# Kernel tuning notes

Hardware: AMD Instinct MI355X
Metric: run time of the kernel (lower is better)

## Reference

```python
import jax, jax.numpy as jnp
import numpy as np

B, N, D, H = 2, 2048, 1024, 16
HD = D // H
SCALE = 1.0 / float(np.sqrt(HD))


def _cx(r, i):
    return (r + 1j * i).astype(jnp.complex64)


def setup_inputs() -> dict:
    key = jax.random.key(0)
    ks = jax.random.split(key, 20)
    inp = {
        "Z_r": jax.random.normal(ks[0], (B, N, D), jnp.float32),
        "Z_i": jax.random.normal(ks[1], (B, N, D), jnp.float32),
    }
    i = 2
    w_scale = 0.02
    for nm in ("q", "k", "v", "o"):
        inp[f"w{nm}_r"] = jax.random.normal(ks[i], (D, D), jnp.float32) * w_scale
        inp[f"w{nm}_i"] = jax.random.normal(ks[i + 1], (D, D), jnp.float32) * w_scale
        inp[f"b{nm}_r"] = jax.random.normal(ks[i + 2], (D,), jnp.float32) * w_scale
        inp[f"b{nm}_i"] = jax.random.normal(ks[i + 3], (D,), jnp.float32) * w_scale
        i += 4
    inp["mask"] = jax.random.randint(ks[18], (B, N), 0, 2, jnp.int32)
    return inp


def reference(Z_r, Z_i, wq_r, wq_i, bq_r, bq_i, wk_r, wk_i, bk_r, bk_i,
              wv_r, wv_i, bv_r, bv_i, wo_r, wo_i, bo_r, bo_i, mask):
    Z = _cx(Z_r, Z_i)  # (B,N,D) complex64

    def lin(x, wr, wi, br, bi):  # complex nn.Linear: x @ W^T + b
        return x @ _cx(wr, wi).T + _cx(br, bi)

    def heads(x):  # (B,N,D) -> (B,H,N,HD)
        return x.reshape(B, N, H, HD).transpose(0, 2, 1, 3)

    q = heads(lin(Z, wq_r, wq_i, bq_r, bq_i))
    k = heads(lin(Z, wk_r, wk_i, bk_r, bk_i))
    v = heads(lin(Z, wv_r, wv_i, bv_r, bv_i))

    # Re(q @ k^T) with plain transpose (no conjugate), as in the torch code:
    # Re = qr.kr^T - qi.ki^T  (computed directly on real parts, no wasted imag GEMM)
    scores = (jnp.einsum('bhnd,bhmd->bhnm', q.real, k.real)
              - jnp.einsum('bhnd,bhmd->bhnm', q.imag, k.imag)) * SCALE
    scores = jnp.where(mask[:, None, None, :] == 0, jnp.float32(-1e9), scores)
    w = jax.nn.softmax(scores, axis=-1)  # (B,H,N,N) real

    # complex output: real weights times complex V -> apply to real/imag separately
    out_r = jnp.einsum('bhnm,bhmd->bhnd', w, v.real)
    out_i = jnp.einsum('bhnm,bhmd->bhnd', w, v.imag)
    out = _cx(out_r, out_i).transpose(0, 2, 1, 3).reshape(B, N, D)

    y = Z + lin(out, wo_r, wo_i, bo_r, bo_i)
    # return real/imag stacked as float32: (2,B,N,D)
    return jnp.stack([y.real, y.imag])
```

## Files before the change

kernel.cpp:

```cpp
#include <hip/hip_runtime.h>
#include <math.h>

#define BB 2
#define NN 2048
#define DD 1024
#define KA 2048
#define HH 16
#define HD 64
#define MM (BB*NN)
#define SCALE 0.125f

typedef __attribute__((ext_vector_type(8))) short bf16x8;
typedef __attribute__((ext_vector_type(4))) short bf16x4;
typedef __attribute__((ext_vector_type(4))) float f32x4;

#define MFMA(a,b,c) __builtin_amdgcn_mfma_f32_16x16x32_bf16(a,b,c,0,0,0)

__device__ __forceinline__ unsigned short f2bf(float x) {
    union { float f; unsigned u; } v; v.f = x;
    unsigned r = v.u + 0x7FFFu + ((v.u >> 16) & 1u);
    return (unsigned short)(r >> 16);
}

__device__ __forceinline__ void async16(void* l, const void* g) {
    __builtin_amdgcn_global_load_lds(
        (const __attribute__((address_space(1))) unsigned int*)g,
        (__attribute__((address_space(3))) unsigned int*)l, 16, 0, 0);
}

__device__ __forceinline__ bf16x8 ld8s(const short* p) {
    bf16x4 lo = *(const bf16x4*)p;
    bf16x4 hi = *(const bf16x4*)(p + 4);
    bf16x8 r;
    r[0]=lo[0]; r[1]=lo[1]; r[2]=lo[2]; r[3]=lo[3];
    r[4]=hi[0]; r[5]=hi[1]; r[6]=hi[2]; r[7]=hi[3];
    return r;
}
__device__ __forceinline__ void st8s(short* p, bf16x8 v) {
    bf16x4 lo, hi;
    lo[0]=v[0]; lo[1]=v[1]; lo[2]=v[2]; lo[3]=v[3];
    hi[0]=v[4]; hi[1]=v[5]; hi[2]=v[6]; hi[3]=v[7];
    *(bf16x4*)p = lo;
    *(bf16x4*)(p + 4) = hi;
}

__global__ __launch_bounds__(256) void mask_scan(const int* __restrict__ mask,
                                                 int* __restrict__ idxArr,
                                                 int* __restrict__ cntArr)
{
    const int b = blockIdx.x, t = threadIdx.x;
    __shared__ int part[256];
    int m[8]; int c = 0;
#pragma unroll
    for (int j = 0; j < 8; j++) { m[j] = mask[b*NN + t*8 + j]; c += (m[j] != 0); }
    part[t] = c; __syncthreads();
    for (int off = 1; off < 256; off <<= 1) {
        int v = (t >= off) ? part[t - off] : 0;
        __syncthreads();
        part[t] += v;
        __syncthreads();
    }
    int base = part[t] - c;
    int total = part[255];
#pragma unroll
    for (int j = 0; j < 8; j++) if (m[j]) idxArr[b*NN + base++] = t*8 + j;
    for (int p = total + t; p < NN; p += 256) idxArr[b*NN + p] = 0;
    if (t == 0) cntArr[b] = total;
}

__global__ __launch_bounds__(256) void cvt_aug(
    const float* __restrict__ Zr, const float* __restrict__ Zi,
    const float* __restrict__ wqr, const float* __restrict__ wqi,
    const float* __restrict__ wkr, const float* __restrict__ wki,
    const float* __restrict__ wvr, const float* __restrict__ wvi,
    const float* __restrict__ wor, const float* __restrict__ woi,
    unsigned short* __restrict__ Zaug,
    unsigned short* __restrict__ Wqa, unsigned short* __restrict__ Wka,
    unsigned short* __restrict__ Wva, unsigned short* __restrict__ Woa)
{
    const int bid = blockIdx.x, t = threadIdx.x;
    const int col = t * 8;
    const float* src;
    float sgn = 1.0f;
    unsigned short* dst;

    if (bid < 4096) {
        const int m = bid;
        src = (col < 1024) ? (Zr + (size_t)m*1024 + col) : (Zi + (size_t)m*1024 + col - 1024);
        dst = Zaug + (size_t)m * KA + col;
    } else {
        const int w = (bid - 4096) >> 11;
        const int r = (bid - 4096) & 2047;
        const int o = r & 1023;
        const float *wr_, *wi_;
        unsigned short* wa;
        switch (w) {
            case 0: wr_ = wqr; wi_ = wqi; wa = Wqa; break;
            case 1: wr_ = wkr; wi_ = wki; wa = Wka; break;
            case 2: wr_ = wvr; wi_ = wvi; wa = Wva; break;
            default: wr_ = wor; wi_ = woi; wa = Woa; break;
        }
        const bool imagrow = (r >= 1024);
        if (!imagrow) {
            if (col < 1024) { src = wr_ + (size_t)o*1024 + col; sgn = 1.0f; }
            else            { src = wi_ + (size_t)o*1024 + col - 1024; sgn = -1.0f; }
        } else {
            const float s = (w == 1) ? -1.0f : 1.0f;
            if (col < 1024) { src = wi_ + (size_t)o*1024 + col; sgn = s; }
            else            { src = wr_ + (size_t)o*1024 + col - 1024; sgn = s; }
        }
        dst = wa + (size_t)r * KA + col;
    }

    float4 a = *(const float4*)src;
    float4 b4 = *(const float4*)(src + 4);
    bf16x8 o8;
    o8[0]=(short)f2bf(sgn*a.x); o8[1]=(short)f2bf(sgn*a.y);
    o8[2]=(short)f2bf(sgn*a.z); o8[3]=(short)f2bf(sgn*a.w);
    o8[4]=(short)f2bf(sgn*b4.x); o8[5]=(short)f2bf(sgn*b4.y);
    o8[6]=(short)f2bf(sgn*b4.z); o8[7]=(short)f2bf(sgn*b4.w);
    *(bf16x8*)dst = o8;
}

__global__ __launch_bounds__(256) void proj_all(
    const unsigned short* __restrict__ Zaug,
    const unsigned short* __restrict__ Wqa, const unsigned short* __restrict__ Wka,
    const unsigned short* __restrict__ Wva,
    const float* __restrict__ bqr, const float* __restrict__ bqi,
    const float* __restrict__ bkr, const float* __restrict__ bki,
    const float* __restrict__ bvr, const float* __restrict__ bvi,
    const int* __restrict__ idxArr, const int* __restrict__ cntArr,
    unsigned short* __restrict__ Qr, unsigned short* __restrict__ Qi,
    unsigned short* __restrict__ Krc, unsigned short* __restrict__ nKic,
    unsigned short* __restrict__ Vtr, unsigned short* __restrict__ Vti)
{
    const int gx = blockIdx.x;
    int slice, b = 0, m0c;
    const unsigned short* wsel;
    const float *br, *bi;
    if (gx < 32) {
        slice = 0; m0c = gx * 128;
        wsel = Wqa; br = bqr; bi = bqi;
    } else if (gx < 64) {
        slice = 1; int t = gx - 32; b = t >> 4; m0c = (t & 15) * 128;
        wsel = Wka; br = bkr; bi = bki;
    } else {
        slice = 2; int t = gx - 64; b = t >> 4; m0c = (t & 15) * 128;
        wsel = Wva; br = bvr; bi = bvi;
    }
    if (slice != 0) {
        const int cnt = cntArr[b];
        if (m0c >= ((cnt + 63) & ~63)) return;
    }

    __shared__ __align__(16) short S[2][128][32];
    __shared__ int idx_s[128];

    const int tid = threadIdx.x;
    const int lane = tid & 63, wave = tid >> 6;
    const int lr = lane & 15, lg = lane >> 4;
    const int wrow = (wave >> 1) * 64, wcol = (wave & 1) * 64;
    const int o0 = blockIdx.y * 128;

    if (tid < 128)
        idx_s[tid] = (slice == 0) ? (m0c + tid) : (b*NN + idxArr[b*NN + m0c + tid]);
    __syncthreads();

    const int rsub = lane >> 2;
    const int colo = (lane & 3) * 8;

    const unsigned short* gp[4];
    gp[0] = Zaug + (size_t)idx_s[wave*16 + rsub] * KA + colo;
    gp[1] = Zaug + (size_t)idx_s[(wave + 4)*16 + rsub] * KA + colo;
    gp[2] = wsel + (size_t)(o0 + wave*16 + rsub) * KA + colo;
    gp[3] = wsel + (size_t)(o0 + 64 + wave*16 + rsub) * KA + colo;

    char* lp[4];
    lp[0] = (char*)S + (size_t)wave * 1024 + (size_t)lane * 16;
    lp[1] = (char*)S + (size_t)(wave + 4) * 1024 + (size_t)lane * 16;
    lp[2] = (char*)S + 8192 + (size_t)wave * 1024 + (size_t)lane * 16;
    lp[3] = (char*)S + 8192 + (size_t)(wave + 4) * 1024 + (size_t)lane * 16;

    f32x4 acc[4][4];
#pragma unroll
    for (int m = 0; m < 4; m++)
#pragma unroll
        for (int n = 0; n < 4; n++) acc[m][n] = (f32x4){0.f,0.f,0.f,0.f};

    for (int k0 = 0; k0 < KA; k0 += 32) {
        __syncthreads();
#pragma unroll
        for (int i = 0; i < 4; i++) {
            async16(lp[i], gp[i]);
            gp[i] += 32;
        }
        __syncthreads();

        bf16x8 af[4], bf[4];
#pragma unroll
        for (int m = 0; m < 4; m++) af[m] = *(const bf16x8*)&S[0][wrow + m*16 + lr][lg*8];
#pragma unroll
        for (int n = 0; n < 4; n++) bf[n] = *(const bf16x8*)&S[1][wcol + n*16 + lr][lg*8];
#pragma unroll
        for (int m = 0; m < 4; m++)
#pragma unroll
            for (int n = 0; n < 4; n++) acc[m][n] = MFMA(af[m], bf[n], acc[m][n]);
    }

#pragma unroll
    for (int mi = 0; mi < 4; mi++)
#pragma unroll
        for (int nj = 0; nj < 4; nj++) {
            const int o = o0 + wcol + nj*16 + lr;
            const int half = o >> 10;
            const int oc = o & 1023;
            const int h = oc >> 6, hd = oc & 63;
            const float bias = half ? ((slice == 1) ? -bi[oc] : bi[oc]) : br[oc];
            if (slice == 2) {
                bf16x4 p4;
#pragma unroll
                for (int reg = 0; reg < 4; reg++)
                    p4[reg] = (short)f2bf(acc[mi][nj][reg] + bias);
                const int jc = m0c + wrow + mi*16 + lg*4;
                size_t base = ((size_t)((b*HH + h)*HD + hd)) * NN + jc;
                if (half) *(bf16x4*)&Vti[base] = p4;
                else      *(bf16x4*)&Vtr[base] = p4;
            } else if (slice == 1) {
                unsigned short* dst = half ? nKic : Krc;
#pragma unroll
                for (int reg = 0; reg < 4; reg++) {
                    const int jc = m0c + wrow + mi*16 + lg*4 + reg;
                    dst[((size_t)((b*HH + h)*NN + jc)) * HD + hd] =
                        f2bf(acc[mi][nj][reg] + bias);
                }
            } else {
                unsigned short* dst = half ? Qi : Qr;
#pragma unroll
                for (int reg = 0; reg < 4; reg++) {
                    const int m = m0c + wrow + mi*16 + lg*4 + reg;
                    const int b2 = m >> 11, n = m & (NN - 1);
                    dst[((size_t)((b2*HH + h)*NN + n)) * HD + hd] =
                        f2bf((acc[mi][nj][reg] + bias) * SCALE);
                }
            }
        }
}

#define LDP 72
__global__ __launch_bounds__(256) void attn_mfma(
    const unsigned short* __restrict__ Qr, const unsigned short* __restrict__ Qi,
    const unsigned short* __restrict__ Krc, const unsigned short* __restrict__ nKic,
    const unsigned short* __restrict__ Vtc, const unsigned short* __restrict__ Vtic,
    const int* __restrict__ cntArr,
    unsigned short* __restrict__ Aaug)
{
    __shared__ short Kr_s[64][LDP], Ki_s[64][LDP], Vr_s[64][LDP], Vi_s[64][LDP];
    __shared__ short P_s[4][32][LDP];

    const int tid = threadIdx.x;
    const int lane = tid & 63, wave = tid >> 6;
    const int lr = lane & 15, lg = lane >> 4;
    const int h = blockIdx.y, b = blockIdx.z;
    const int n0 = blockIdx.x * 128 + wave * 32;
    const size_t qb = ((size_t)(b*HH + h)) * NN * HD;
    const int cnt = cntArr[b];
    const int ct = (cnt + 63) & ~63;

    bf16x8 qr[2][2], qi[2][2];
#pragma unroll
    for (int mf = 0; mf < 2; mf++)
#pragma unroll
        for (int kf = 0; kf < 2; kf++) {
            qr[mf][kf] = *(const bf16x8*)&Qr[qb + (size_t)(n0 + mf*16 + lr) * HD + kf*32 + lg*8];
            qi[mf][kf] = *(const bf16x8*)&Qi[qb + (size_t)(n0 + mf*16 + lr) * HD + kf*32 + lg*8];
        }

    f32x4 o_r[2][4], o_i[2][4];
#pragma unroll
    for (int mf = 0; mf < 2; mf++)
#pragma unroll
        for (int nf = 0; nf < 4; nf++) {
            o_r[mf][nf] = (f32x4){0.f,0.f,0.f,0.f};
            o_i[mf][nf] = (f32x4){0.f,0.f,0.f,0.f};
        }
    float m_run[2][4], l_run[2][4];
#pragma unroll
    for (int mf = 0; mf < 2; mf++)
#pragma unroll
        for (int r = 0; r < 4; r++) { m_run[mf][r] = -3.0e38f; l_run[mf][r] = 0.0f; }

    for (int t0 = 0; t0 < ct; t0 += 64) {
        __syncthreads();
        for (int c = tid; c < 512; c += 256) {
            int row = c >> 3, ch = (c & 7) * 8;
            st8s(&Kr_s[row][ch], *(const bf16x8*)&Krc [qb + (size_t)(t0 + row) * HD + ch]);
            st8s(&Ki_s[row][ch], *(const bf16x8*)&nKic[qb + (size_t)(t0 + row) * HD + ch]);
            st8s(&Vr_s[row][ch], *(const bf16x8*)&Vtc [qb + (size_t)row * NN + t0 + ch]);
            st8s(&Vi_s[row][ch], *(const bf16x8*)&Vtic[qb + (size_t)row * NN + t0 + ch]);
        }
        __syncthreads();

        f32x4 sacc[2][4];
#pragma unroll
        for (int nf = 0; nf < 4; nf++) {
            bf16x8 k0f = ld8s(&Kr_s[nf*16 + lr][lg*8]);
            bf16x8 k1f = ld8s(&Kr_s[nf*16 + lr][32 + lg*8]);
            bf16x8 i0f = ld8s(&Ki_s[nf*16 + lr][lg*8]);
            bf16x8 i1f = ld8s(&Ki_s[nf*16 + lr][32 + lg*8]);
#pragma unroll
            for (int mf = 0; mf < 2; mf++) {
                f32x4 a = (f32x4){0.f,0.f,0.f,0.f};
                a = MFMA(qr[mf][0], k0f, a);
                a = MFMA(qr[mf][1], k1f, a);
                a = MFMA(qi[mf][0], i0f, a);
                a = MFMA(qi[mf][1], i1f, a);
                sacc[mf][nf] = a;
            }
        }

        if (t0 + 64 > cnt) {
#pragma unroll
            for (int nf = 0; nf < 4; nf++) {
                if (t0 + nf*16 + lr >= cnt) {
#pragma unroll
                    for (int mf = 0; mf < 2; mf++)
#pragma unroll
                        for (int r = 0; r < 4; r++) sacc[mf][nf][r] = -1e9f;
                }
            }
        }

#pragma unroll
        for (int mf = 0; mf < 2; mf++) {
            float fac[4];
#pragma unroll
            for (int r = 0; r < 4; r++) {
                float v = fmaxf(fmaxf(sacc[mf][0][r], sacc[mf][1][r]),
                                fmaxf(sacc[mf][2][r], sacc[mf][3][r]));
                v = fmaxf(v, __shfl_xor(v, 1, 64));
                v = fmaxf(v, __shfl_xor(v, 2, 64));
                v = fmaxf(v, __shfl_xor(v, 4, 64));
                v = fmaxf(v, __shfl_xor(v, 8, 64));
                float mn = fmaxf(m_run[mf][r], v);
                fac[r] = __expf(m_run[mf][r] - mn);
                m_run[mf][r] = mn;
            }
            float psum[4] = {0.f, 0.f, 0.f, 0.f};
#pragma unroll
            for (int nf = 0; nf < 4; nf++)
#pragma unroll
                for (int r = 0; r < 4; r++) {
                    float p = __expf(sacc[mf][nf][r] - m_run[mf][r]);
                    psum[r] += p;
                    P_s[wave][mf*16 + lg*4 + r][nf*16 + lr] = (short)f2bf(p);
                }
#pragma unroll
            for (int r = 0; r < 4; r++) {
                float ps = psum[r];
                ps += __shfl_xor(ps, 1, 64);
                ps += __shfl_xor(ps, 2, 64);
                ps += __shfl_xor(ps, 4, 64);
                ps += __shfl_xor(ps, 8, 64);
                l_run[mf][r] = l_run[mf][r] * fac[r] + ps;
            }
#pragma unroll
            for (int nf = 0; nf < 4; nf++)
#pragma unroll
                for (int r = 0; r < 4; r++) {
                    o_r[mf][nf][r] *= fac[r];
                    o_i[mf][nf][r] *= fac[r];
                }
        }
        __syncthreads();

        bf16x8 pa[2][2];
#pragma unroll
        for (int mf = 0; mf < 2; mf++) {
            pa[mf][0] = ld8s(&P_s[wave][mf*16 + lr][lg*8]);
            pa[mf][1] = ld8s(&P_s[wave][mf*16 + lr][32 + lg*8]);
        }
#pragma unroll
        for (int nf = 0; nf < 4; nf++) {
            bf16x8 v0 = ld8s(&Vr_s[nf*16 + lr][lg*8]);
            bf16x8 v1 = ld8s(&Vr_s[nf*16 + lr][32 + lg*8]);
            bf16x8 w0 = ld8s(&Vi_s[nf*16 + lr][lg*8]);
            bf16x8 w1 = ld8s(&Vi_s[nf*16 + lr][32 + lg*8]);
#pragma unroll
            for (int mf = 0; mf < 2; mf++) {
                o_r[mf][nf] = MFMA(pa[mf][0], v0, o_r[mf][nf]);
                o_r[mf][nf] = MFMA(pa[mf][1], v1, o_r[mf][nf]);
                o_i[mf][nf] = MFMA(pa[mf][0], w0, o_i[mf][nf]);
                o_i[mf][nf] = MFMA(pa[mf][1], w1, o_i[mf][nf]);
            }
        }
    }

#pragma unroll
    for (int mf = 0; mf < 2; mf++) {
        float invl[4];
#pragma unroll
        for (int r = 0; r < 4; r++) invl[r] = 1.0f / l_run[mf][r];
#pragma unroll
        for (int nf = 0; nf < 4; nf++)
#pragma unroll
            for (int r = 0; r < 4; r++) {
                int row = n0 + mf*16 + lg*4 + r;
                int col = h*HD + nf*16 + lr;
                size_t o = ((size_t)(b*NN + row)) * KA + col;
                Aaug[o]        = f2bf(o_r[mf][nf][r] * invl[r]);
                Aaug[o + 1024] = f2bf(o_i[mf][nf][r] * invl[r]);
            }
    }
}

__global__ __launch_bounds__(256) void final_mfma(
    const unsigned short* __restrict__ Aaug, const unsigned short* __restrict__ Woa,
    const float* __restrict__ bor, const float* __restrict__ boi,
    const float* __restrict__ Zr, const float* __restrict__ Zi,
    float* __restrict__ out)
{
    __shared__ __align__(16) short S[2][128][32];

    const int tid = threadIdx.x;
    const int lane = tid & 63, wave = tid >> 6;
    const int lr = lane & 15, lg = lane >> 4;
    const int wrow = (wave >> 1) * 64, wcol = (wave & 1) * 64;
    const int m0 = blockIdx.x * 128, o0 = blockIdx.y * 128;

    const int rsub = lane >> 2;
    const int colo = (lane & 3) * 8;

    const unsigned short* gp[4];
    gp[0] = Aaug + (size_t)(m0 + wave*16 + rsub) * KA + colo;
    gp[1] = Aaug + (size_t)(m0 + 64 + wave*16 + rsub) * KA + colo;
    gp[2] = Woa + (size_t)(o0 + wave*16 + rsub) * KA + colo;
    gp[3] = Woa + (size_t)(o0 + 64 + wave*16 + rsub) * KA + colo;

    char* lp[4];
    lp[0] = (char*)S + (size_t)wave * 1024 + (size_t)lane * 16;
    lp[1] = (char*)S + (size_t)(wave + 4) * 1024 + (size_t)lane * 16;
    lp[2] = (char*)S + 8192 + (size_t)wave * 1024 + (size_t)lane * 16;
    lp[3] = (char*)S + 8192 + (size_t)(wave + 4) * 1024 + (size_t)lane * 16;

    f32x4 acc[4][4];
#pragma unroll
    for (int m = 0; m < 4; m++)
#pragma unroll
        for (int n = 0; n < 4; n++) acc[m][n] = (f32x4){0.f,0.f,0.f,0.f};

    for (int k0 = 0; k0 < KA; k0 += 32) {
        __syncthreads();
#pragma unroll
        for (int i = 0; i < 4; i++) {
            async16(lp[i], gp[i]);
            gp[i] += 32;
        }
        __syncthreads();

        bf16x8 af[4], bf[4];
#pragma unroll
        for (int m = 0; m < 4; m++) af[m] = *(const bf16x8*)&S[0][wrow + m*16 + lr][lg*8];
#pragma unroll
        for (int n = 0; n < 4; n++) bf[n] = *(const bf16x8*)&S[1][wcol + n*16 + lr][lg*8];
#pragma unroll
        for (int m = 0; m < 4; m++)
#pragma unroll
            for (int n = 0; n < 4; n++) acc[m][n] = MFMA(af[m], bf[n], acc[m][n]);
    }

#pragma unroll
    for (int mi = 0; mi < 4; mi++)
#pragma unroll
        for (int nj = 0; nj < 4; nj++) {
            const int o = o0 + wcol + nj*16 + lr;
            const int half = o >> 10;
            const int oc = o & 1023;
            const float bias = half ? boi[oc] : bor[oc];
            const float* resid = half ? Zi : Zr;
            float* dst = out + (half ? (size_t)MM * DD : 0);
#pragma unroll
            for (int reg = 0; reg < 4; reg++) {
                const int m = m0 + wrow + mi*16 + lg*4 + reg;
                size_t zi = (size_t)m * DD + oc;
                dst[zi] = acc[mi][nj][reg] + bias + resid[zi];
            }
        }
}

extern "C" void kernel_launch(void* const* d_in, const int* in_sizes, int n_in,
                              void* d_out, int out_size, void* d_ws, size_t ws_size,
                              hipStream_t stream)
{
    const float* Zr  = (const float*)d_in[0];
    const float* Zi  = (const float*)d_in[1];
    const float* wqr = (const float*)d_in[2];
    const float* wqi = (const float*)d_in[3];
    const float* bqr = (const float*)d_in[4];
    const float* bqi = (const float*)d_in[5];
    const float* wkr = (const float*)d_in[6];
    const float* wki = (const float*)d_in[7];
    const float* bkr = (const float*)d_in[8];
    const float* bki = (const float*)d_in[9];
    const float* wvr = (const float*)d_in[10];
    const float* wvi = (const float*)d_in[11];
    const float* bvr = (const float*)d_in[12];
    const float* bvi = (const float*)d_in[13];
    const float* wor = (const float*)d_in[14];
    const float* woi = (const float*)d_in[15];
    const float* bor = (const float*)d_in[16];
    const float* boi = (const float*)d_in[17];
    const int*  mask = (const int*)d_in[18];

    unsigned short* w16 = (unsigned short*)d_ws;
    const size_t ZA = (size_t)MM * KA;
    const size_t WA = (size_t)KA * KA;
    const size_t HN = (size_t)MM * DD;
    unsigned short* Zaug = w16;
    unsigned short* Wqa  = Zaug + ZA;
    unsigned short* Wka  = Wqa + WA;
    unsigned short* Wva  = Wka + WA;
    unsigned short* Woa  = Wva + WA;
    unsigned short* Qr16 = Woa + WA;
    unsigned short* Qi16 = Qr16 + HN;
    unsigned short* Krc16 = Qi16 + HN;
    unsigned short* nKic16 = Krc16 + HN;
    unsigned short* Vtr16 = nKic16 + HN;
    unsigned short* Vti16 = Vtr16 + HN;
    unsigned short* Aaug = Vti16 + HN;
    int* idxArr = (int*)(Aaug + ZA);
    int* cntArr = idxArr + BB * NN;

    mask_scan<<<BB, 256, 0, stream>>>(mask, idxArr, cntArr);

    cvt_aug<<<12288, 256, 0, stream>>>(
        Zr, Zi, wqr, wqi, wkr, wki, wvr, wvi, wor, woi,
        Zaug, Wqa, Wka, Wva, Woa);

    proj_all<<<dim3(96, 16), 256, 0, stream>>>(
        Zaug, Wqa, Wka, Wva,
        bqr, bqi, bkr, bki, bvr, bvi, idxArr, cntArr,
        Qr16, Qi16, Krc16, nKic16, Vtr16, Vti16);

    attn_mfma<<<dim3(NN/128, HH, BB), 256, 0, stream>>>(
        Qr16, Qi16, Krc16, nKic16, Vtr16, Vti16, cntArr, Aaug);

    final_mfma<<<dim3(32, 16), 256, 0, stream>>>(
        Aaug, Woa, bor, boi, Zr, Zi, (float*)d_out);
}
```

Baseline: 298.5 us.

## Double-buffer LDS tiles in projection and output GEMM kernels

Both the QKV projection GEMM and the final output-projection GEMM now use two LDS buffers. The async global-to-LDS copy for the next K-slice is issued before the MFMAs on the current slice, and there is a single wait-plus-barrier per iteration instead of two barriers around a blocking load. This is meant to hide global load latency behind matrix math, at the cost of doubling the GEMM shared memory to 32 KB per block, which may reduce occupancy. The last iteration issues a prefetch one slice past the K extent, which reads slightly beyond each row and, for the final row, possibly past the allocation.

After: 309.5 us. 1.04x slower.

```diff
diff --git a/kernel.cpp b/kernel.cpp
--- a/kernel.cpp
+++ b/kernel.cpp
@@ -153,7 +153,7 @@
         if (m0c >= ((cnt + 63) & ~63)) return;
     }
 
-    __shared__ __align__(16) short S[2][128][32];
+    __shared__ __align__(16) short S[2][2][128][32];
     __shared__ int idx_s[128];
 
     const int tid = threadIdx.x;
@@ -175,11 +175,11 @@
     gp[2] = wsel + (size_t)(o0 + wave*16 + rsub) * KA + colo;
     gp[3] = wsel + (size_t)(o0 + 64 + wave*16 + rsub) * KA + colo;
 
-    char* lp[4];
-    lp[0] = (char*)S + (size_t)wave * 1024 + (size_t)lane * 16;
-    lp[1] = (char*)S + (size_t)(wave + 4) * 1024 + (size_t)lane * 16;
-    lp[2] = (char*)S + 8192 + (size_t)wave * 1024 + (size_t)lane * 16;
-    lp[3] = (char*)S + 8192 + (size_t)(wave + 4) * 1024 + (size_t)lane * 16;
+    int lpo[4];
+    lpo[0] = wave * 1024 + lane * 16;
+    lpo[1] = (wave + 4) * 1024 + lane * 16;
+    lpo[2] = 8192 + wave * 1024 + lane * 16;
+    lpo[3] = 8192 + (wave + 4) * 1024 + lane * 16;
 
     f32x4 acc[4][4];
 #pragma unroll
@@ -187,24 +187,33 @@
 #pragma unroll
         for (int n = 0; n < 4; n++) acc[m][n] = (f32x4){0.f,0.f,0.f,0.f};
 
-    for (int k0 = 0; k0 < KA; k0 += 32) {
-        __syncthreads();
-#pragma unroll
-        for (int i = 0; i < 4; i++) {
-            async16(lp[i], gp[i]);
-            gp[i] += 32;
-        }
-        __syncthreads();
-
-        bf16x8 af[4], bf[4];
-#pragma unroll
-        for (int m = 0; m < 4; m++) af[m] = *(const bf16x8*)&S[0][wrow + m*16 + lr][lg*8];
-#pragma unroll
-        for (int n = 0; n < 4; n++) bf[n] = *(const bf16x8*)&S[1][wcol + n*16 + lr][lg*8];
+#pragma unroll
+    for (int i = 0; i < 4; i++) { async16((char*)S + lpo[i], gp[i]); gp[i] += 32; }
+    asm volatile("s_waitcnt vmcnt(0)" ::: "memory");
+    __builtin_amdgcn_s_barrier();
+    __builtin_amdgcn_sched_barrier(0);
+
+    for (int t = 0; t < KA/32; t++) {
+        const int cur = t & 1;
+        char* nb = (char*)S + (cur ^ 1) * 16384;
+#pragma unroll
+        for (int i = 0; i < 4; i++) { async16(nb + lpo[i], gp[i]); gp[i] += 32; }
+
+        const short (*Sa)[32] = (const short (*)[32])((const char*)S + cur * 16384);
+        const short (*Sb)[32] = Sa + 128;
+        bf16x8 af[4], bw[4];
+#pragma unroll
+        for (int m = 0; m < 4; m++) af[m] = *(const bf16x8*)&Sa[wrow + m*16 + lr][lg*8];
+#pragma unroll
+        for (int n = 0; n < 4; n++) bw[n] = *(const bf16x8*)&Sb[wcol + n*16 + lr][lg*8];
 #pragma unroll
         for (int m = 0; m < 4; m++)
 #pragma unroll
-            for (int n = 0; n < 4; n++) acc[m][n] = MFMA(af[m], bf[n], acc[m][n]);
+            for (int n = 0; n < 4; n++) acc[m][n] = MFMA(af[m], bw[n], acc[m][n]);
+
+        asm volatile("s_waitcnt vmcnt(0)" ::: "memory");
+        __builtin_amdgcn_s_barrier();
+        __builtin_amdgcn_sched_barrier(0);
     }
 
 #pragma unroll
@@ -419,7 +428,7 @@
     const float* __restrict__ Zr, const float* __restrict__ Zi,
     float* __restrict__ out)
 {
-    __shared__ __align__(16) short S[2][128][32];
+    __shared__ __align__(16) short S[2][2][128][32];
 
     const int tid = threadIdx.x;
     const int lane = tid & 63, wave = tid >> 6;
@@ -436,11 +445,11 @@
     gp[2] = Woa + (size_t)(o0 + wave*16 + rsub) * KA + colo;
     gp[3] = Woa + (size_t)(o0 + 64 + wave*16 + rsub) * KA + colo;
 
-    char* lp[4];
-    lp[0] = (char*)S + (size_t)wave * 1024 + (size_t)lane * 16;
-    lp[1] = (char*)S + (size_t)(wave + 4) * 1024 + (size_t)lane * 16;
-    lp[2] = (char*)S + 8192 + (size_t)wave * 1024 + (size_t)lane * 16;
-    lp[3] = (char*)S + 8192 + (size_t)(wave + 4) * 1024 + (size_t)lane * 16;
+    int lpo[4];
+    lpo[0] = wave * 1024 + lane * 16;
+    lpo[1] = (wave + 4) * 1024 + lane * 16;
+    lpo[2] = 8192 + wave * 1024 + lane * 16;
+    lpo[3] = 8192 + (wave + 4) * 1024 + lane * 16;
 
     f32x4 acc[4][4];
 #pragma unroll
@@ -448,24 +457,33 @@
 #pragma unroll
         for (int n = 0; n < 4; n++) acc[m][n] = (f32x4){0.f,0.f,0.f,0.f};
 
-    for (int k0 = 0; k0 < KA; k0 += 32) {
-        __syncthreads();
-#pragma unroll
-        for (int i = 0; i < 4; i++) {
-            async16(lp[i], gp[i]);
-            gp[i] += 32;
-        }
-        __syncthreads();
-
-        bf16x8 af[4], bf[4];
-#pragma unroll
-        for (int m = 0; m < 4; m++) af[m] = *(const bf16x8*)&S[0][wrow + m*16 + lr][lg*8];
-#pragma unroll
-        for (int n = 0; n < 4; n++) bf[n] = *(const bf16x8*)&S[1][wcol + n*16 + lr][lg*8];
+#pragma unroll
+    for (int i = 0; i < 4; i++) { async16((char*)S + lpo[i], gp[i]); gp[i] += 32; }
+    asm volatile("s_waitcnt vmcnt(0)" ::: "memory");
+    __builtin_amdgcn_s_barrier();
+    __builtin_amdgcn_sched_barrier(0);
+
+    for (int t = 0; t < KA/32; t++) {
+        const int cur = t & 1;
+        char* nb = (char*)S + (cur ^ 1) * 16384;
+#pragma unroll
+        for (int i = 0; i < 4; i++) { async16(nb + lpo[i], gp[i]); gp[i] += 32; }
+
+        const short (*Sa)[32] = (const short (*)[32])((const char*)S + cur * 16384);
+        const short (*Sb)[32] = Sa + 128;
+        bf16x8 af[4], bw[4];
+#pragma unroll
+        for (int m = 0; m < 4; m++) af[m] = *(const bf16x8*)&Sa[wrow + m*16 + lr][lg*8];
+#pragma unroll
+        for (int n = 0; n < 4; n++) bw[n] = *(const bf16x8*)&Sb[wcol + n*16 + lr][lg*8];
 #pragma unroll
         for (int m = 0; m < 4; m++)
 #pragma unroll
-            for (int n = 0; n < 4; n++) acc[m][n] = MFMA(af[m], bf[n], acc[m][n]);
+            for (int n = 0; n < 4; n++) acc[m][n] = MFMA(af[m], bw[n], acc[m][n]);
+
+        asm volatile("s_waitcnt vmcnt(0)" ::: "memory");
+        __builtin_amdgcn_s_barrier();
+        __builtin_amdgcn_sched_barrier(0);
     }
 
 #pragma unroll
```
